# Kernel tuning notes

Measured on AMD Instinct MI355X. Metric: run time of the kernel, lower is better.

The kernel has to match this reference:

```python
import jax, jax.numpy as jnp
import numpy as np

B, S, H, E, K, NH = 2, 2048, 1024, 8, 2, 8
HD = H // NH          # head dim = 128
HQ = H // 4           # seasonal encoder width = 256
CAP = int(B * S * 1.5 * K / E)  # expert capacity = 1536


def setup_inputs() -> dict:
    key = jax.random.key(0)
    ks = iter(jax.random.split(key, 32))

    def lin(shape):
        fan_in = shape[0]
        return jax.random.normal(next(ks), shape, jnp.float32) / np.sqrt(fan_in)

    inp = {
        "hidden_states": jax.random.normal(next(ks), (B, S, H), jnp.float32),
        # position embedding table [sequence_length, H]
        "pos_emb": jax.random.normal(next(ks), (S, H), jnp.float32) * 0.02,
        # temporal_encoder: Linear(H+2,H) -> ReLU -> Linear(H,H)
        "We1": lin((H + 2, H)), "be1": jnp.zeros((H,), jnp.float32),
        "We2": lin((H, H)),     "be2": jnp.zeros((H,), jnp.float32),
        # seasonal_encoder: Linear(1,H//4) -> ReLU -> Linear(H//4,H//4)
        "Ws1": lin((1, HQ)),   "bs1": jnp.zeros((HQ,), jnp.float32),
        "Ws2": lin((HQ, HQ)),  "bs2": jnp.zeros((HQ,), jnp.float32),
        # temporal_attention (MultiheadAttention, 8 heads)
        "Wq": lin((H, H)), "bq": jnp.zeros((H,), jnp.float32),
        "Wk": lin((H, H)), "bk": jnp.zeros((H,), jnp.float32),
        "Wv": lin((H, H)), "bv": jnp.zeros((H,), jnp.float32),
        "Wo": lin((H, H)), "bo": jnp.zeros((H,), jnp.float32),
        # temporal_router: Linear(H,H) -> ReLU -> Linear(H,E)
        "Wr1": lin((H, H)), "br1": jnp.zeros((H,), jnp.float32),
        "Wr2": lin((H, E)), "br2": jnp.zeros((E,), jnp.float32),
    }
    return inp


def _forward(hidden_states, pos_emb, We1, be1, We2, be2, Ws1, bs1, Ws2, bs2,
             Wq, bq, Wk, bk, Wv, bv, Wo, bo, Wr1, br1, Wr2, br2):
    b, s, h = hidden_states.shape
    # time features (time_info is None -> defaults)
    t = jnp.arange(s, dtype=jnp.float32)                   # [S]
    season = jnp.sin(t * 2.0 * jnp.pi / 24.0)              # [S]
    time_feat = jnp.broadcast_to(jnp.stack([t, season], -1), (b, s, 2))

    combined = jnp.concatenate([hidden_states, time_feat], axis=-1)  # [B,S,H+2]
    enc = jax.nn.relu(combined @ We1 + be1) @ We2 + be2              # [B,S,H]

    pos = pos_emb[:s]                                                # [S,H]
    seas = jax.nn.relu(season[:, None] @ Ws1 + bs1) @ Ws2 + bs2      # [S,H//4]
    seas_full = jnp.tile(seas, (1, h // seas.shape[-1]))             # [S,H] (expand to H)

    x = enc + pos[None] + seas_full[None]                            # [B,S,H]

    # self-attention (eval mode, no dropout)
    def heads(y):
        return y.reshape(b, s, NH, HD)
    q = heads(x @ Wq + bq)
    k = heads(x @ Wk + bk)
    v = heads(x @ Wv + bv)
    scores = jnp.einsum('bqhd,bkhd->bhqk', q, k) / np.sqrt(HD)
    attn = jax.nn.softmax(scores, axis=-1)
    ctx = jnp.einsum('bhqk,bkhd->bqhd', attn, v).reshape(b, s, h)
    x = ctx @ Wo + bo

    logits = jax.nn.relu(x @ Wr1 + br1) @ Wr2 + br2                  # [B,S,E]
    probs = jax.nn.softmax(logits, axis=-1)

    topv, topi = jax.lax.top_k(probs, K)                             # [B,S,K]
    topv = topv / topv.sum(-1, keepdims=True)

    onehot = jax.nn.one_hot(topi, E, dtype=probs.dtype)              # [B,S,K,E]
    disp0 = onehot.sum(-2)                                           # [B,S,E] (0/1)
    comb0 = (topv[..., None] * onehot).sum(-2)                       # [B,S,E]

    # only capacity slot 0 is ever written (per original code)
    dispatch = jnp.zeros((b, s, E, CAP), probs.dtype).at[..., 0].set(disp0)
    combine = jnp.zeros((b, s, E, CAP), probs.dtype).at[..., 0].set(comb0)

    p_mean = probs.mean(axis=(0, 1))                                 # [E]
    aux_loss = jnp.sum(p_mean * jnp.log(p_mean * E + 1e-9))
    return dispatch, combine, probs, aux_loss


def reference(hidden_states, pos_emb, We1, be1, We2, be2, Ws1, bs1, Ws2, bs2,
              Wq, bq, Wk, bk, Wv, bv, Wo, bo, Wr1, br1, Wr2, br2):
    return _forward(hidden_states, pos_emb, We1, be1, We2, be2, Ws1, bs1, Ws2, bs2,
                    Wq, bq, Wk, bk, Wv, bv, Wo, bo, Wr1, br1, Wr2, br2)
```

## Files before the change

### kernel.cpp

```cpp
#include <hip/hip_runtime.h>
#include <hip/hip_fp16.h>
#include <math.h>

#define N_TOK 4096
#define S_LEN 2048
#define H_DIM 1024
#define E_EXP 8
#define CAPV  1536
#define NHEAD 8
#define HDHD  128

#define SCRATCH_F4 2129920u
#define TOTAL_F4   25165824u

typedef __attribute__((ext_vector_type(8))) _Float16 v8h;
typedef __attribute__((ext_vector_type(4))) float v4f;

__device__ __forceinline__ void splitf16(float v, unsigned short& h, unsigned short& l) {
    __half hh = __float2half(v);
    h = __half_as_ushort(hh);
    l = __half_as_ushort(__float2half(v - __half2float(hh)));
}

__device__ __forceinline__ void gld_lds16(const void* g, void* l) {
    __builtin_amdgcn_global_load_lds(
        (const __attribute__((address_space(1))) unsigned int*)g,
        (__attribute__((address_space(3))) unsigned int*)l,
        16, 0, 0);
}

__global__ __launch_bounds__(256) void prep_k(
    const float* __restrict__ hid, unsigned short* __restrict__ hi,
    unsigned short* __restrict__ lo,
    const float* __restrict__ Ws1, const float* __restrict__ bs1,
    const float* __restrict__ Ws2, const float* __restrict__ bs2,
    float* __restrict__ seasons, float* __restrict__ seas24,
    const float* __restrict__ Wr2, float* __restrict__ wr2t) {
    __shared__ float hbuf[256];
    int blk = blockIdx.x;
    int tid = threadIdx.x;
    if (blk < 4096) {
        int i = blk * 256 + tid;
        float4 v = ((const float4*)hid)[i];
        ushort4 h, l;
        splitf16(v.x, h.x, l.x);
        splitf16(v.y, h.y, l.y);
        splitf16(v.z, h.z, l.z);
        splitf16(v.w, h.w, l.w);
        ((ushort4*)hi)[i] = h;
        ((ushort4*)lo)[i] = l;
    } else if (blk < 4104) {
        int s = (blk - 4096) * 256 + tid;
        if (s < S_LEN) {
            double a = (double)s * 2.0 * M_PI / 24.0;
            seasons[s] = (float)sin(a);
        }
    } else if (blk < 4128) {
        int m = blk - 4104;
        double a = (double)m * 2.0 * M_PI / 24.0;
        float sv = (float)sin(a);
        int j = tid;
        hbuf[j] = fmaxf(sv * Ws1[j] + bs1[j], 0.f);
        __syncthreads();
        float acc = bs2[j];
        for (int i = 0; i < 256; ++i) acc = fmaf(hbuf[i], Ws2[i * 256 + j], acc);
        seas24[m * 256 + j] = acc;
    } else {
        int i = (blk - 4128) * 256 + tid;
        int k = i >> 3, e = i & 7;
        wr2t[e * 1024 + k] = Wr2[i];
    }
}

__device__ __forceinline__ void wconv_body(const float* __restrict__ W,
                                           unsigned short* __restrict__ Thi,
                                           unsigned short* __restrict__ Tlo) {
    __shared__ unsigned short Hs[64][65];
    __shared__ unsigned short Ls[64][65];
    int k0 = blockIdx.y * 64, n0 = blockIdx.x * 64;
    int tid = threadIdx.x;
#pragma unroll
    for (int i = 0; i < 4; ++i) {
        int idx = tid + i * 256;
        int kk = idx >> 4, n4 = idx & 15;
        float4 v = *(const float4*)(W + (size_t)(k0 + kk) * 1024 + n0 + n4 * 4);
        unsigned short h, l;
        splitf16(v.x, h, l); Hs[n4 * 4 + 0][kk] = h; Ls[n4 * 4 + 0][kk] = l;
        splitf16(v.y, h, l); Hs[n4 * 4 + 1][kk] = h; Ls[n4 * 4 + 1][kk] = l;
        splitf16(v.z, h, l); Hs[n4 * 4 + 2][kk] = h; Ls[n4 * 4 + 2][kk] = l;
        splitf16(v.w, h, l); Hs[n4 * 4 + 3][kk] = h; Ls[n4 * 4 + 3][kk] = l;
    }
    __syncthreads();
#pragma unroll
    for (int i = 0; i < 4; ++i) {
        int idx = tid + i * 256;
        int n = idx >> 4, k4 = idx & 15;
        ushort4 h = make_ushort4(Hs[n][k4 * 4], Hs[n][k4 * 4 + 1], Hs[n][k4 * 4 + 2], Hs[n][k4 * 4 + 3]);
        ushort4 l = make_ushort4(Ls[n][k4 * 4], Ls[n][k4 * 4 + 1], Ls[n][k4 * 4 + 2], Ls[n][k4 * 4 + 3]);
        *(ushort4*)(Thi + (size_t)(n0 + n) * 1024 + k0 + k4 * 4) = h;
        *(ushort4*)(Tlo + (size_t)(n0 + n) * 1024 + k0 + k4 * 4) = l;
    }
}

struct WBatch {
    const float* src[7];
    unsigned short* dh[7];
    unsigned short* dl[7];
};

__global__ __launch_bounds__(256) void wconv_batch_k(WBatch wb) {
    int i = blockIdx.z;
    wconv_body(wb.src[i], wb.dh[i], wb.dl[i]);
}

__device__ __forceinline__ void fill_body(float* __restrict__ p, size_t f40, size_t f41, int nblk) {
    v4f z = {0.f, 0.f, 0.f, 0.f};
    v4f* o = (v4f*)p;
    size_t n = f41 - f40;
    size_t T = blockDim.x;
    for (size_t i = (size_t)blockIdx.x * T + threadIdx.x; i < n; i += (size_t)nblk * T)
        __builtin_nontemporal_store(z, o + f40 + i);
}

template <int MODE, int EMITF, int EMITS, int FILLN>
__global__ __launch_bounds__(512, 4) void gemm_split(
    const unsigned short* __restrict__ Ahi, const unsigned short* __restrict__ Alo,
    const unsigned short* __restrict__ WThi, const unsigned short* __restrict__ WTlo,
    const float* __restrict__ bias, float* __restrict__ Cf,
    unsigned short* __restrict__ Chi, unsigned short* __restrict__ Clo,
    const float* __restrict__ rowT, const float* __restrict__ rowS,
    const float* __restrict__ seasons, const float* __restrict__ pos,
    const float* __restrict__ seas24, float escale, float* __restrict__ fillp) {
    if (FILLN > 0) {
        if (blockIdx.x < (unsigned)FILLN) {
            fill_body(fillp, 0, SCRATCH_F4, FILLN);
            return;
        }
    }
    __shared__ unsigned short Ash[2][128 * 32];
    __shared__ unsigned short Asl[2][128 * 32];
    __shared__ unsigned short Bsh[2][128 * 32];
    __shared__ unsigned short Bsl[2][128 * 32];
    int tid = threadIdx.x;
    int lane = tid & 63, w = tid >> 6;
    int l15 = lane & 15, l16 = lane >> 4;
    int wm = (w >> 1) * 32, wn = (w & 1) * 64;

    int bid = blockIdx.x - FILLN;
    int mp = (bid & 7) + ((bid >> 6) << 3);
    int np = (bid >> 3) & 7;
    int m0 = mp * 128, n0 = np * 128;

    int ac0 = tid;
    int ar0 = ac0 >> 2;
    size_t a_src0 = (size_t)(m0 + ar0) * 1024 + (((ac0 & 3) ^ (ar0 & 3)) * 8);
    size_t b_src0 = (size_t)(n0 + ar0) * 1024 + (((ac0 & 3) ^ (ar0 & 3)) * 8);

    int a_off[2], b_off[4];
#pragma unroll
    for (int mi = 0; mi < 2; ++mi) {
        int row = wm + mi * 16 + l15;
        a_off[mi] = row * 32 + ((l16 ^ (row & 3)) * 8);
    }
#pragma unroll
    for (int ni = 0; ni < 4; ++ni) {
        int n = wn + ni * 16 + l15;
        b_off[ni] = n * 32 + ((l16 ^ (n & 3)) * 8);
    }

    auto STAGE = [&](int buf, int k0) {
        gld_lds16(Ahi + a_src0 + k0, &Ash[buf][ac0 * 8]);
        gld_lds16(Alo + a_src0 + k0, &Asl[buf][ac0 * 8]);
        gld_lds16(WThi + b_src0 + k0, &Bsh[buf][ac0 * 8]);
        gld_lds16(WTlo + b_src0 + k0, &Bsl[buf][ac0 * 8]);
    };

    v4f acc[2][4] = {};
    STAGE(0, 0);
    __syncthreads();

    for (int kk = 0; kk < 32; ++kk) {
        int cur = kk & 1;
        if (kk < 31) STAGE(cur ^ 1, (kk + 1) * 32);
        v8h ah[2], al[2], bh[4], bl[4];
#pragma unroll
        for (int mi = 0; mi < 2; ++mi) {
            ah[mi] = *(const v8h*)&Ash[cur][a_off[mi]];
            al[mi] = *(const v8h*)&Asl[cur][a_off[mi]];
        }
#pragma unroll
        for (int ni = 0; ni < 4; ++ni) {
            bh[ni] = *(const v8h*)&Bsh[cur][b_off[ni]];
            bl[ni] = *(const v8h*)&Bsl[cur][b_off[ni]];
        }
#pragma unroll
        for (int mi = 0; mi < 2; ++mi)
#pragma unroll
            for (int ni = 0; ni < 4; ++ni) {
                acc[mi][ni] = __builtin_amdgcn_mfma_f32_16x16x32_f16(ah[mi], bh[ni], acc[mi][ni], 0, 0, 0);
                acc[mi][ni] = __builtin_amdgcn_mfma_f32_16x16x32_f16(al[mi], bh[ni], acc[mi][ni], 0, 0, 0);
                acc[mi][ni] = __builtin_amdgcn_mfma_f32_16x16x32_f16(ah[mi], bl[ni], acc[mi][ni], 0, 0, 0);
            }
        __syncthreads();
    }

#pragma unroll
    for (int mi = 0; mi < 2; ++mi) {
#pragma unroll
        for (int r = 0; r < 4; ++r) {
            int row = m0 + wm + mi * 16 + l16 * 4 + r;
            int s = row & (S_LEN - 1);
            float tval = 0.f, seval = 0.f;
            if (MODE == 1) { tval = (float)s; seval = seasons[s]; }
#pragma unroll
            for (int ni = 0; ni < 4; ++ni) {
                int col = n0 + wn + ni * 16 + l15;
                float v = acc[mi][ni][r] + bias[col];
                if (MODE == 1) v += tval * rowT[col] + seval * rowS[col];
                if (MODE == 2) v += pos[(size_t)s * 1024 + col] + seas24[(s % 24) * 256 + (col & 255)];
                if (MODE == 1 || MODE == 3) v = fmaxf(v, 0.f);
                size_t o = (size_t)row * 1024 + col;
                if (EMITF) Cf[o] = v;
                if (EMITS) {
                    unsigned short hu, lu;
                    splitf16(v * escale, hu, lu);
                    Chi[o] = hu; Clo[o] = lu;
                }
            }
        }
    }
}

#define NFILLQ 128
__global__ __launch_bounds__(512, 4) void gemm_qkv(
    const unsigned short* __restrict__ Ahi, const unsigned short* __restrict__ Alo,
    const unsigned short* __restrict__ WT3hi, const unsigned short* __restrict__ WT3lo,
    const float* __restrict__ bq, const float* __restrict__ bk,
    const float* __restrict__ bv,
    unsigned short* __restrict__ Qhi, unsigned short* __restrict__ Qlo,
    unsigned short* __restrict__ Khi, unsigned short* __restrict__ Klo,
    unsigned short* __restrict__ VThi, unsigned short* __restrict__ VTlo,
    float qscale, float* __restrict__ fillp) {
    if (blockIdx.x < NFILLQ) {
        fill_body(fillp, SCRATCH_F4, TOTAL_F4, NFILLQ);
        return;
    }
    __shared__ unsigned short Ash[2][128 * 32];
    __shared__ unsigned short Asl[2][128 * 32];
    __shared__ unsigned short Bsh[2][128 * 32];
    __shared__ unsigned short Bsl[2][128 * 32];
    int tid = threadIdx.x;
    int lane = tid & 63, w = tid >> 6;
    int l15 = lane & 15, l16 = lane >> 4;
    int wm = (w >> 1) * 32, wn = (w & 1) * 64;

    int bid = blockIdx.x - NFILLQ;
    int t = bid >> 3;
    int np = t % 24;
    int mp = (bid & 7) + (t / 24) * 8;
    int m0 = mp * 128;
    int wn0 = np * 128;

    int ac0 = tid;
    int ar0 = ac0 >> 2;
    size_t a_src0 = (size_t)(m0 + ar0) * 1024 + (((ac0 & 3) ^ (ar0 & 3)) * 8);
    size_t b_src0 = (size_t)(wn0 + ar0) * 1024 + (((ac0 & 3) ^ (ar0 & 3)) * 8);

    int a_off[2], b_off[4];
#pragma unroll
    for (int mi = 0; mi < 2; ++mi) {
        int row = wm + mi * 16 + l15;
        a_off[mi] = row * 32 + ((l16 ^ (row & 3)) * 8);
    }
#pragma unroll
    for (int ni = 0; ni < 4; ++ni) {
        int n = wn + ni * 16 + l15;
        b_off[ni] = n * 32 + ((l16 ^ (n & 3)) * 8);
    }

    auto STAGE = [&](int buf, int k0) {
        gld_lds16(Ahi + a_src0 + k0, &Ash[buf][ac0 * 8]);
        gld_lds16(Alo + a_src0 + k0, &Asl[buf][ac0 * 8]);
        gld_lds16(WT3hi + b_src0 + k0, &Bsh[buf][ac0 * 8]);
        gld_lds16(WT3lo + b_src0 + k0, &Bsl[buf][ac0 * 8]);
    };

    v4f acc[2][4] = {};
    STAGE(0, 0);
    __syncthreads();

    for (int kk = 0; kk < 32; ++kk) {
        int cur = kk & 1;
        if (kk < 31) STAGE(cur ^ 1, (kk + 1) * 32);
        v8h ah[2], al[2], bh[4], bl[4];
#pragma unroll
        for (int mi = 0; mi < 2; ++mi) {
            ah[mi] = *(const v8h*)&Ash[cur][a_off[mi]];
            al[mi] = *(const v8h*)&Asl[cur][a_off[mi]];
        }
#pragma unroll
        for (int ni = 0; ni < 4; ++ni) {
            bh[ni] = *(const v8h*)&Bsh[cur][b_off[ni]];
            bl[ni] = *(const v8h*)&Bsl[cur][b_off[ni]];
        }
#pragma unroll
        for (int mi = 0; mi < 2; ++mi)
#pragma unroll
            for (int ni = 0; ni < 4; ++ni) {
                acc[mi][ni] = __builtin_amdgcn_mfma_f32_16x16x32_f16(ah[mi], bh[ni], acc[mi][ni], 0, 0, 0);
                acc[mi][ni] = __builtin_amdgcn_mfma_f32_16x16x32_f16(al[mi], bh[ni], acc[mi][ni], 0, 0, 0);
                acc[mi][ni] = __builtin_amdgcn_mfma_f32_16x16x32_f16(ah[mi], bl[ni], acc[mi][ni], 0, 0, 0);
            }
        __syncthreads();
    }

    if (np >= 16) {
        int n0 = (np - 16) * 128;
#pragma unroll
        for (int mi = 0; mi < 2; ++mi) {
            int row0 = m0 + wm + mi * 16 + l16 * 4;
            int bb = row0 >> 11, ss = row0 & 2047;
#pragma unroll
            for (int ni = 0; ni < 4; ++ni) {
                int col = n0 + wn + ni * 16 + l15;
                int hh = col >> 7, dd = col & 127;
                size_t base = ((size_t)((bb * 8 + hh) * 128 + dd)) * 2048 + ss;
                ushort4 vh, vl;
                float v0 = acc[mi][ni][0] + bv[col];
                float v1 = acc[mi][ni][1] + bv[col];
                float v2 = acc[mi][ni][2] + bv[col];
                float v3 = acc[mi][ni][3] + bv[col];
                splitf16(v0, vh.x, vl.x);
                splitf16(v1, vh.y, vl.y);
                splitf16(v2, vh.z, vl.z);
                splitf16(v3, vh.w, vl.w);
                *(ushort4*)(VThi + base) = vh;
                *(ushort4*)(VTlo + base) = vl;
            }
        }
    } else {
        const float* bias = np < 8 ? bq : bk;
        unsigned short* Dhi = np < 8 ? Qhi : Khi;
        unsigned short* Dlo = np < 8 ? Qlo : Klo;
        float esc = np < 8 ? qscale : 1.f;
        int n0 = (np & 7) * 128;
#pragma unroll
        for (int mi = 0; mi < 2; ++mi) {
#pragma unroll
            for (int r = 0; r < 4; ++r) {
                int row = m0 + wm + mi * 16 + l16 * 4 + r;
#pragma unroll
                for (int ni = 0; ni < 4; ++ni) {
                    int col = n0 + wn + ni * 16 + l15;
                    float v = (acc[mi][ni][r] + bias[col]) * esc;
                    size_t o = (size_t)row * 1024 + col;
                    unsigned short hu, lu;
                    splitf16(v, hu, lu);
                    Dhi[o] = hu; Dlo[o] = lu;
                }
            }
        }
    }
}

__global__ __launch_bounds__(256, 4) void attn_mfma_k(
    const unsigned short* __restrict__ qhi, const unsigned short* __restrict__ qlo,
    const unsigned short* __restrict__ khi, const unsigned short* __restrict__ klo,
    const unsigned short* __restrict__ vthi, const unsigned short* __restrict__ vtlo,
    float* __restrict__ OP, float* __restrict__ ML) {
    __shared__ unsigned short Ks_hi[32 * 128];
    __shared__ unsigned short Ks_lo[32 * 128];
    __shared__ unsigned short Vs_hi[128 * 32];
    __shared__ unsigned short Vs_lo[128 * 32];
    __shared__ unsigned int   Ps[64 * 32];

    int p = blockIdx.x;
    int x = (p >> 3) & 31;
    int g = (p & 7) + ((p >> 8) << 3);
    int bh = g >> 1, z = g & 1;
    int b = bh >> 3, h = bh & 7;
    int q0 = x * 64;
    int tid = threadIdx.x;
    int lane = tid & 63, w = tid >> 6;
    int l15 = lane & 15, l16 = lane >> 4;
    int wm = w * 16;

    v8h qa_h[4], qa_l[4];
    {
        size_t qrow = (size_t)(b * S_LEN + q0 + wm + l15) * H_DIM + h * HDHD;
#pragma unroll
        for (int ks = 0; ks < 4; ++ks) {
            qa_h[ks] = *(const v8h*)(qhi + qrow + ks * 32 + l16 * 8);
            qa_l[ks] = *(const v8h*)(qlo + qrow + ks * 32 + l16 * 8);
        }
    }

    int ktok1 = tid >> 4, kslot1 = tid & 15;
    int ktok2 = ktok1 + 16;
    size_t ksrc1 = (size_t)(b * S_LEN + ktok1) * H_DIM + h * HDHD + ((kslot1 ^ (ktok1 & 7)) * 8);
    size_t ksrc2 = (size_t)(b * S_LEN + ktok2) * H_DIM + h * HDHD + ((kslot1 ^ (ktok2 & 7)) * 8);
    int vd1 = tid >> 2, vslot1 = tid & 3;
    int vd2 = vd1 + 64;
    size_t vsrc1 = (size_t)(bh * HDHD + vd1) * S_LEN + ((vslot1 ^ ((vd1 >> 1) & 3)) * 8);
    size_t vsrc2 = (size_t)(bh * HDHD + vd2) * S_LEN + ((vslot1 ^ ((vd2 >> 1) & 3)) * 8);

    v4f accO[8] = {};
    float mreg[4] = {-1e30f, -1e30f, -1e30f, -1e30f};
    float lreg[4] = {};

    int kt0 = z * 1024;
    for (int it = 0; it < 32; ++it) {
        int kt = kt0 + it * 32;
        __syncthreads();
        size_t koff = (size_t)kt * H_DIM;
        gld_lds16(khi + ksrc1 + koff, &Ks_hi[tid * 8]);
        gld_lds16(khi + ksrc2 + koff, &Ks_hi[(tid + 256) * 8]);
        gld_lds16(klo + ksrc1 + koff, &Ks_lo[tid * 8]);
        gld_lds16(klo + ksrc2 + koff, &Ks_lo[(tid + 256) * 8]);
        gld_lds16(vthi + vsrc1 + kt, &Vs_hi[tid * 8]);
        gld_lds16(vthi + vsrc2 + kt, &Vs_hi[(tid + 256) * 8]);
        gld_lds16(vtlo + vsrc1 + kt, &Vs_lo[tid * 8]);
        gld_lds16(vtlo + vsrc2 + kt, &Vs_lo[(tid + 256) * 8]);
        __syncthreads();

        v4f s0 = {}, s1 = {};
#pragma unroll
        for (int ks = 0; ks < 4; ++ks) {
#pragma unroll
            for (int nt = 0; nt < 2; ++nt) {
                int tok = nt * 16 + l15;
                int slot = (ks * 4 + l16) ^ (tok & 7);
                v8h bhf = *(const v8h*)&Ks_hi[tok * 128 + slot * 8];
                v8h blf = *(const v8h*)&Ks_lo[tok * 128 + slot * 8];
                v4f& ss = nt ? s1 : s0;
                ss = __builtin_amdgcn_mfma_f32_16x16x32_f16(qa_h[ks], bhf, ss, 0, 0, 0);
                ss = __builtin_amdgcn_mfma_f32_16x16x32_f16(qa_l[ks], bhf, ss, 0, 0, 0);
                ss = __builtin_amdgcn_mfma_f32_16x16x32_f16(qa_h[ks], blf, ss, 0, 0, 0);
            }
        }

        float p0[4], p1[4], alpha[4];
#pragma unroll
        for (int r = 0; r < 4; ++r) {
            float tmax = fmaxf(s0[r], s1[r]);
            tmax = fmaxf(tmax, __shfl_xor(tmax, 1));
            tmax = fmaxf(tmax, __shfl_xor(tmax, 2));
            tmax = fmaxf(tmax, __shfl_xor(tmax, 4));
            tmax = fmaxf(tmax, __shfl_xor(tmax, 8));
            float mnew = fmaxf(mreg[r], tmax);
            alpha[r] = __expf(mreg[r] - mnew);
            p0[r] = __expf(s0[r] - mnew);
            p1[r] = __expf(s1[r] - mnew);
            float lt = p0[r] + p1[r];
            lt += __shfl_xor(lt, 1);
            lt += __shfl_xor(lt, 2);
            lt += __shfl_xor(lt, 4);
            lt += __shfl_xor(lt, 8);
            lreg[r] = lreg[r] * alpha[r] + lt;
            mreg[r] = mnew;
        }
#pragma unroll
        for (int nt = 0; nt < 8; ++nt)
#pragma unroll
            for (int r = 0; r < 4; ++r) accO[nt][r] *= alpha[r];

#pragma unroll
        for (int r = 0; r < 4; ++r) {
            int qq = wm + l16 * 4 + r;
            unsigned short ph, pl;
            splitf16(p0[r], ph, pl);
            int k0i = l15;
            Ps[qq * 32 + ((((k0i >> 2) ^ (qq & 7)) << 2) | (k0i & 3))] =
                (unsigned)ph | ((unsigned)pl << 16);
            splitf16(p1[r], ph, pl);
            int k1i = 16 + l15;
            Ps[qq * 32 + ((((k1i >> 2) ^ (qq & 7)) << 2) | (k1i & 3))] =
                (unsigned)ph | ((unsigned)pl << 16);
        }

        int qq = wm + l15;
        int sA = (l16 * 2) ^ (qq & 7);
        int sB = (l16 * 2 + 1) ^ (qq & 7);
        uint4 ua = *(const uint4*)&Ps[qq * 32 + sA * 4];
        uint4 ub = *(const uint4*)&Ps[qq * 32 + sB * 4];
        uint4 ahw, alw;
        ahw.x = (ua.x & 0xffffu) | (ua.y << 16);
        ahw.y = (ua.z & 0xffffu) | (ua.w << 16);
        ahw.z = (ub.x & 0xffffu) | (ub.y << 16);
        ahw.w = (ub.z & 0xffffu) | (ub.w << 16);
        alw.x = (ua.x >> 16) | (ua.y & 0xffff0000u);
        alw.y = (ua.z >> 16) | (ua.w & 0xffff0000u);
        alw.z = (ub.x >> 16) | (ub.y & 0xffff0000u);
        alw.w = (ub.z >> 16) | (ub.w & 0xffff0000u);
        v8h pA_h = __builtin_bit_cast(v8h, ahw);
        v8h pA_l = __builtin_bit_cast(v8h, alw);
#pragma unroll
        for (int nt = 0; nt < 8; ++nt) {
            int d = nt * 16 + l15;
            int slot = l16 ^ ((d >> 1) & 3);
            v8h vhf = *(const v8h*)&Vs_hi[d * 32 + slot * 8];
            v8h vlf = *(const v8h*)&Vs_lo[d * 32 + slot * 8];
            accO[nt] = __builtin_amdgcn_mfma_f32_16x16x32_f16(pA_h, vhf, accO[nt], 0, 0, 0);
            accO[nt] = __builtin_amdgcn_mfma_f32_16x16x32_f16(pA_l, vhf, accO[nt], 0, 0, 0);
            accO[nt] = __builtin_amdgcn_mfma_f32_16x16x32_f16(pA_h, vlf, accO[nt], 0, 0, 0);
        }
    }

#pragma unroll
    for (int r = 0; r < 4; ++r) {
        if (l15 == 0) {
            int q = q0 + wm + l16 * 4 + r;
            size_t mlo = ((size_t)(z * 16 + bh) * 2048 + q) * 2;
            ML[mlo] = mreg[r];
            ML[mlo + 1] = lreg[r];
        }
    }
#pragma unroll
    for (int nt = 0; nt < 8; ++nt) {
#pragma unroll
        for (int r = 0; r < 4; ++r) {
            int q = q0 + wm + l16 * 4 + r;
            size_t o = ((size_t)(z * 16 + bh) * 2048 + q) * 128 + nt * 16 + l15;
            OP[o] = accO[nt][r];
        }
    }
}

__global__ __launch_bounds__(256) void attn_combine_k(
    const float* __restrict__ OP, const float* __restrict__ ML,
    unsigned short* __restrict__ ctx_hi, unsigned short* __restrict__ ctx_lo) {
    int tid = threadIdx.x;
    int R = blockIdx.x * 16 + (tid >> 4);
    int bh = R >> 11, q = R & 2047;
    int b = bh >> 3, h = bh & 7;
    int d0 = (tid & 15) * 8;
    size_t ml0 = ((size_t)bh * 2048 + q) * 2;
    size_t ml1 = ((size_t)(16 + bh) * 2048 + q) * 2;
    float m0 = ML[ml0], l0 = ML[ml0 + 1];
    float m1 = ML[ml1], l1 = ML[ml1 + 1];
    float m = fmaxf(m0, m1);
    float w0 = __expf(m0 - m), w1 = __expf(m1 - m);
    float inv = 1.f / (w0 * l0 + w1 * l1);
    const float* O0 = OP + ((size_t)bh * 2048 + q) * 128 + d0;
    const float* O1 = OP + ((size_t)(16 + bh) * 2048 + q) * 128 + d0;
    size_t dst = ((size_t)(b * 2048 + q)) * 1024 + h * 128 + d0;
    float4 a0 = *(const float4*)O0;
    float4 a1 = *(const float4*)(O0 + 4);
    float4 c0 = *(const float4*)O1;
    float4 c1 = *(const float4*)(O1 + 4);
    ushort4 h0, h1, lo0, lo1;
    splitf16((w0 * a0.x + w1 * c0.x) * inv, h0.x, lo0.x);
    splitf16((w0 * a0.y + w1 * c0.y) * inv, h0.y, lo0.y);
    splitf16((w0 * a0.z + w1 * c0.z) * inv, h0.z, lo0.z);
    splitf16((w0 * a0.w + w1 * c0.w) * inv, h0.w, lo0.w);
    splitf16((w0 * a1.x + w1 * c1.x) * inv, h1.x, lo1.x);
    splitf16((w0 * a1.y + w1 * c1.y) * inv, h1.y, lo1.y);
    splitf16((w0 * a1.z + w1 * c1.z) * inv, h1.z, lo1.z);
    splitf16((w0 * a1.w + w1 * c1.w) * inv, h1.w, lo1.w);
    *(ushort4*)(ctx_hi + dst) = h0;
    *(ushort4*)(ctx_hi + dst + 4) = h1;
    *(ushort4*)(ctx_lo + dst) = lo0;
    *(ushort4*)(ctx_lo + dst + 4) = lo1;
}

__global__ __launch_bounds__(256) void logits_topk_k(const float* __restrict__ h1,
                                                     const float* __restrict__ Wr2T,
                                                     const float* __restrict__ br2,
                                                     float* __restrict__ out) {
    __shared__ float part[256];
    __shared__ float lg[8][8];
    int tid = threadIdx.x;
    int tok8 = tid >> 5;
    int e = (tid >> 2) & 7;
    int ch = tid & 3;
    int tok = blockIdx.x * 8 + tok8;
    const float4* h4 = (const float4*)(h1 + (size_t)tok * 1024 + ch * 256);
    const float4* w4 = (const float4*)(Wr2T + (size_t)e * 1024 + ch * 256);
    float acc = 0.f;
#pragma unroll
    for (int i = 0; i < 64; ++i) {
        float4 a = h4[i];
        float4 bb = w4[i];
        acc = fmaf(a.x, bb.x, fmaf(a.y, bb.y, fmaf(a.z, bb.z, fmaf(a.w, bb.w, acc))));
    }
    part[tid] = acc;
    __syncthreads();
    if (ch == 0)
        lg[tok8][e] = part[tid] + part[tid + 1] + part[tid + 2] + part[tid + 3] + br2[e];
    __syncthreads();
    if (tid < 8) {
        int myTok = blockIdx.x * 8 + tid;
        float l[8], p[8];
        float mx = -1e30f;
#pragma unroll
        for (int k = 0; k < 8; ++k) { l[k] = lg[tid][k]; mx = fmaxf(mx, l[k]); }
        float sum = 0.f;
#pragma unroll
        for (int k = 0; k < 8; ++k) { p[k] = __expf(l[k] - mx); sum += p[k]; }
        float inv = 1.f / sum;
#pragma unroll
        for (int k = 0; k < 8; ++k) p[k] *= inv;
        const size_t NEC = (size_t)N_TOK * E_EXP * CAPV;
        float* probs_out = out + 2 * NEC;
#pragma unroll
        for (int k = 0; k < 8; ++k) probs_out[(size_t)myTok * 8 + k] = p[k];
        int i1 = 0;
#pragma unroll
        for (int k = 1; k < 8; ++k) if (p[k] > p[i1]) i1 = k;
        int i2 = -1;
#pragma unroll
        for (int k = 0; k < 8; ++k) {
            if (k == i1) continue;
            if (i2 < 0 || p[k] > p[i2]) i2 = k;
        }
        float v1 = p[i1], v2 = p[i2], tv = v1 + v2;
        size_t base = (size_t)myTok * E_EXP * CAPV;
        out[base + (size_t)i1 * CAPV] = 1.f;
        out[base + (size_t)i2 * CAPV] = 1.f;
        out[NEC + base + (size_t)i1 * CAPV] = v1 / tv;
        out[NEC + base + (size_t)i2 * CAPV] = v2 / tv;
    }
}

__global__ void aux_k(const float* __restrict__ probs, float* __restrict__ out_aux) {
    __shared__ float part[256];
    int tid = threadIdx.x;
    int e = tid & 7, chunk = tid >> 3;
    float s = 0.f;
    for (int t = chunk * 128; t < (chunk + 1) * 128; ++t)
        s += probs[(size_t)t * 8 + e];
    part[tid] = s;
    __syncthreads();
    if (tid < 8) {
        float tot = 0.f;
        for (int c = 0; c < 32; ++c) tot += part[c * 8 + e];
        part[tid] = tot / (float)N_TOK;
    }
    __syncthreads();
    if (tid == 0) {
        float aux = 0.f;
        for (int e2 = 0; e2 < 8; ++e2) {
            float pm = part[e2];
            aux += pm * logf(pm * 8.f + 1e-9f);
        }
        *out_aux = aux;
    }
}

extern "C" void kernel_launch(void* const* d_in, const int* in_sizes, int n_in,
                              void* d_out, int out_size, void* d_ws, size_t ws_size,
                              hipStream_t stream) {
    const float* hid = (const float*)d_in[0];
    const float* pos = (const float*)d_in[1];
    const float* We1 = (const float*)d_in[2];
    const float* be1 = (const float*)d_in[3];
    const float* We2 = (const float*)d_in[4];
    const float* be2 = (const float*)d_in[5];
    const float* Ws1 = (const float*)d_in[6];
    const float* bs1 = (const float*)d_in[7];
    const float* Ws2 = (const float*)d_in[8];
    const float* bs2 = (const float*)d_in[9];
    const float* Wq  = (const float*)d_in[10]; const float* bq = (const float*)d_in[11];
    const float* Wk  = (const float*)d_in[12]; const float* bk = (const float*)d_in[13];
    const float* Wv  = (const float*)d_in[14]; const float* bv = (const float*)d_in[15];
    const float* Wo  = (const float*)d_in[16]; const float* bo = (const float*)d_in[17];
    const float* Wr1 = (const float*)d_in[18]; const float* br1 = (const float*)d_in[19];
    const float* Wr2 = (const float*)d_in[20]; const float* br2 = (const float*)d_in[21];

    float* out = (float*)d_out;
    char* base = (char*)d_ws;
    const size_t AC  = (size_t)N_TOK * H_DIM;
    const size_t SPC = AC * 2;
    const size_t FB  = AC * 4;
    const size_t MB  = (size_t)1 << 20;

    unsigned short* B1hi = (unsigned short*)(base);
    unsigned short* B1lo = (unsigned short*)(base + SPC);
    unsigned short* B2hi = (unsigned short*)(base + FB);
    unsigned short* B2lo = (unsigned short*)(base + FB + SPC);
    unsigned short* Qhi  = (unsigned short*)(base + 2 * FB);
    unsigned short* Qlo  = (unsigned short*)(base + 2 * FB + SPC);
    unsigned short* Khi  = (unsigned short*)(base + 3 * FB);
    unsigned short* Klo  = (unsigned short*)(base + 3 * FB + SPC);
    unsigned short* VThi = (unsigned short*)(base + 4 * FB);
    unsigned short* VTlo = (unsigned short*)(base + 4 * FB + SPC);
    float* h1f = (float*)(base + 3 * FB);

    char* wp = base + 5 * FB;
    unsigned short* We1hi = (unsigned short*)(wp);
    unsigned short* We1lo = (unsigned short*)(wp + 2 * MB);
    unsigned short* We2hi = (unsigned short*)(wp + 4 * MB);
    unsigned short* We2lo = (unsigned short*)(wp + 6 * MB);
    unsigned short* QKVhi = (unsigned short*)(wp + 8 * MB);
    unsigned short* QKVlo = (unsigned short*)(wp + 14 * MB);
    unsigned short* Wohi  = (unsigned short*)(wp + 20 * MB);
    unsigned short* Wolo  = (unsigned short*)(wp + 22 * MB);
    unsigned short* Wr1hi = (unsigned short*)(wp + 24 * MB);
    unsigned short* Wr1lo = (unsigned short*)(wp + 26 * MB);
    char* smalls = wp + 28 * MB;
    float* wr2t    = (float*)smalls;
    float* seas24  = wr2t + 8192;
    float* seasons = seas24 + 6144;

    const size_t NEC = (size_t)N_TOK * E_EXP * CAPV;
    const float QSCALE = 0.08838834764831845f;

    float* OP = out;
    float* ML = out + (size_t)2 * 16 * 2048 * 128;

    dim3 blk(256), blk512(512);

    prep_k<<<4160, blk, 0, stream>>>(hid, B1hi, B1lo, Ws1, bs1, Ws2, bs2,
                                     seasons, seas24, Wr2, wr2t);

    WBatch wb;
    wb.src[0] = We1; wb.dh[0] = We1hi; wb.dl[0] = We1lo;
    wb.src[1] = We2; wb.dh[1] = We2hi; wb.dl[1] = We2lo;
    wb.src[2] = Wq;  wb.dh[2] = QKVhi;                        wb.dl[2] = QKVlo;
    wb.src[3] = Wk;  wb.dh[3] = QKVhi + (size_t)1024 * 1024;  wb.dl[3] = QKVlo + (size_t)1024 * 1024;
    wb.src[4] = Wv;  wb.dh[4] = QKVhi + (size_t)2048 * 1024;  wb.dl[4] = QKVlo + (size_t)2048 * 1024;
    wb.src[5] = Wo;  wb.dh[5] = Wohi;  wb.dl[5] = Wolo;
    wb.src[6] = Wr1; wb.dh[6] = Wr1hi; wb.dl[6] = Wr1lo;
    wconv_batch_k<<<dim3(16, 16, 7), blk, 0, stream>>>(wb);

    gemm_split<1, 0, 1, 0><<<256, blk512, 0, stream>>>(B1hi, B1lo, We1hi, We1lo, be1,
        nullptr, B2hi, B2lo,
        We1 + (size_t)1024 * 1024, We1 + (size_t)1025 * 1024, seasons, nullptr, nullptr, 1.f, nullptr);
    gemm_split<2, 0, 1, 0><<<256, blk512, 0, stream>>>(B2hi, B2lo, We2hi, We2lo, be2,
        nullptr, B1hi, B1lo, nullptr, nullptr, nullptr, pos, seas24, 1.f, nullptr);

    gemm_qkv<<<768 + NFILLQ, blk512, 0, stream>>>(B1hi, B1lo, QKVhi, QKVlo, bq, bk, bv,
                                                  Qhi, Qlo, Khi, Klo, VThi, VTlo, QSCALE, out);

    attn_mfma_k<<<1024, blk, 0, stream>>>(Qhi, Qlo, Khi, Klo, VThi, VTlo, OP, ML);
    attn_combine_k<<<2048, blk, 0, stream>>>(OP, ML, B2hi, B2lo);

    gemm_split<0, 0, 1, 32><<<256 + 32, blk512, 0, stream>>>(B2hi, B2lo, Wohi, Wolo, bo,
        nullptr, B1hi, B1lo, nullptr, nullptr, nullptr, nullptr, nullptr, 1.f, out);
    gemm_split<3, 1, 0, 0><<<256, blk512, 0, stream>>>(B1hi, B1lo, Wr1hi, Wr1lo, br1,
        h1f, nullptr, nullptr, nullptr, nullptr, nullptr, nullptr, nullptr, 1.f, nullptr);

    logits_topk_k<<<512, blk, 0, stream>>>(h1f, wr2t, br2, out);
    aux_k<<<1, blk, 0, stream>>>(out + 2 * NEC, out + 2 * NEC + (size_t)N_TOK * E_EXP);
}
```

Before: 523.6 us.

## Merge prep and weight-conversion kernels; enlarge attention query tile to 128

Folds the weight hi/lo split-and-transpose blocks into the prep kernel so both run in a single launch, removing one kernel boundary. The attention kernel now runs 512-thread blocks covering 128 query rows, so each K/V tile staged in LDS is shared by twice as many query rows and each thread issues half as many async loads. The trade-off is fewer blocks (512), lower occupancy per launch bound, and a larger P buffer in shared memory.

```diff
diff --git a/kernel.cpp b/kernel.cpp
--- a/kernel.cpp
+++ b/kernel.cpp
@@ -29,14 +29,21 @@
         16, 0, 0);
 }
 
-__global__ __launch_bounds__(256) void prep_k(
+struct WBatch {
+    const float* src[7];
+    unsigned short* dh[7];
+    unsigned short* dl[7];
+};
+
+__global__ __launch_bounds__(256) void prep_wconv_k(
     const float* __restrict__ hid, unsigned short* __restrict__ hi,
     unsigned short* __restrict__ lo,
     const float* __restrict__ Ws1, const float* __restrict__ bs1,
     const float* __restrict__ Ws2, const float* __restrict__ bs2,
     float* __restrict__ seasons, float* __restrict__ seas24,
-    const float* __restrict__ Wr2, float* __restrict__ wr2t) {
-    __shared__ float hbuf[256];
+    const float* __restrict__ Wr2, float* __restrict__ wr2t, WBatch wb) {
+    __shared__ unsigned short Hs[64][65];
+    __shared__ unsigned short Ls[64][65];
     int blk = blockIdx.x;
     int tid = threadIdx.x;
     if (blk < 4096) {
@@ -56,6 +63,7 @@
             seasons[s] = (float)sin(a);
         }
     } else if (blk < 4128) {
+        float* hbuf = (float*)Hs;
         int m = blk - 4104;
         double a = (double)m * 2.0 * M_PI / 24.0;
         float sv = (float)sin(a);
@@ -65,52 +73,40 @@
         float acc = bs2[j];
         for (int i = 0; i < 256; ++i) acc = fmaf(hbuf[i], Ws2[i * 256 + j], acc);
         seas24[m * 256 + j] = acc;
-    } else {
+    } else if (blk < 4160) {
         int i = (blk - 4128) * 256 + tid;
         int k = i >> 3, e = i & 7;
         wr2t[e * 1024 + k] = Wr2[i];
-    }
-}
-
-__device__ __forceinline__ void wconv_body(const float* __restrict__ W,
-                                           unsigned short* __restrict__ Thi,
-                                           unsigned short* __restrict__ Tlo) {
-    __shared__ unsigned short Hs[64][65];
-    __shared__ unsigned short Ls[64][65];
-    int k0 = blockIdx.y * 64, n0 = blockIdx.x * 64;
-    int tid = threadIdx.x;
-#pragma unroll
-    for (int i = 0; i < 4; ++i) {
-        int idx = tid + i * 256;
-        int kk = idx >> 4, n4 = idx & 15;
-        float4 v = *(const float4*)(W + (size_t)(k0 + kk) * 1024 + n0 + n4 * 4);
-        unsigned short h, l;
-        splitf16(v.x, h, l); Hs[n4 * 4 + 0][kk] = h; Ls[n4 * 4 + 0][kk] = l;
-        splitf16(v.y, h, l); Hs[n4 * 4 + 1][kk] = h; Ls[n4 * 4 + 1][kk] = l;
-        splitf16(v.z, h, l); Hs[n4 * 4 + 2][kk] = h; Ls[n4 * 4 + 2][kk] = l;
-        splitf16(v.w, h, l); Hs[n4 * 4 + 3][kk] = h; Ls[n4 * 4 + 3][kk] = l;
-    }
-    __syncthreads();
-#pragma unroll
-    for (int i = 0; i < 4; ++i) {
-        int idx = tid + i * 256;
-        int n = idx >> 4, k4 = idx & 15;
-        ushort4 h = make_ushort4(Hs[n][k4 * 4], Hs[n][k4 * 4 + 1], Hs[n][k4 * 4 + 2], Hs[n][k4 * 4 + 3]);
-        ushort4 l = make_ushort4(Ls[n][k4 * 4], Ls[n][k4 * 4 + 1], Ls[n][k4 * 4 + 2], Ls[n][k4 * 4 + 3]);
-        *(ushort4*)(Thi + (size_t)(n0 + n) * 1024 + k0 + k4 * 4) = h;
-        *(ushort4*)(Tlo + (size_t)(n0 + n) * 1024 + k0 + k4 * 4) = l;
-    }
-}
-
-struct WBatch {
-    const float* src[7];
-    unsigned short* dh[7];
-    unsigned short* dl[7];
-};
-
-__global__ __launch_bounds__(256) void wconv_batch_k(WBatch wb) {
-    int i = blockIdx.z;
-    wconv_body(wb.src[i], wb.dh[i], wb.dl[i]);
+    } else {
+        int i2 = blk - 4160;
+        int wi = i2 >> 8;
+        int rem = i2 & 255;
+        int k0 = (rem >> 4) << 6, n0 = (rem & 15) << 6;
+        const float* __restrict__ W = wb.src[wi];
+        unsigned short* __restrict__ Thi = wb.dh[wi];
+        unsigned short* __restrict__ Tlo = wb.dl[wi];
+#pragma unroll
+        for (int i = 0; i < 4; ++i) {
+            int idx = tid + i * 256;
+            int kk = idx >> 4, n4 = idx & 15;
+            float4 v = *(const float4*)(W + (size_t)(k0 + kk) * 1024 + n0 + n4 * 4);
+            unsigned short h, l;
+            splitf16(v.x, h, l); Hs[n4 * 4 + 0][kk] = h; Ls[n4 * 4 + 0][kk] = l;
+            splitf16(v.y, h, l); Hs[n4 * 4 + 1][kk] = h; Ls[n4 * 4 + 1][kk] = l;
+            splitf16(v.z, h, l); Hs[n4 * 4 + 2][kk] = h; Ls[n4 * 4 + 2][kk] = l;
+            splitf16(v.w, h, l); Hs[n4 * 4 + 3][kk] = h; Ls[n4 * 4 + 3][kk] = l;
+        }
+        __syncthreads();
+#pragma unroll
+        for (int i = 0; i < 4; ++i) {
+            int idx = tid + i * 256;
+            int n = idx >> 4, k4 = idx & 15;
+            ushort4 h = make_ushort4(Hs[n][k4 * 4], Hs[n][k4 * 4 + 1], Hs[n][k4 * 4 + 2], Hs[n][k4 * 4 + 3]);
+            ushort4 l = make_ushort4(Ls[n][k4 * 4], Ls[n][k4 * 4 + 1], Ls[n][k4 * 4 + 2], Ls[n][k4 * 4 + 3]);
+            *(ushort4*)(Thi + (size_t)(n0 + n) * 1024 + k0 + k4 * 4) = h;
+            *(ushort4*)(Tlo + (size_t)(n0 + n) * 1024 + k0 + k4 * 4) = l;
+        }
+    }
 }
 
 __device__ __forceinline__ void fill_body(float* __restrict__ p, size_t f40, size_t f41, int nblk) {
@@ -363,7 +359,7 @@
     }
 }
 
-__global__ __launch_bounds__(256, 4) void attn_mfma_k(
+__global__ __launch_bounds__(512, 2) void attn_mfma_k(
     const unsigned short* __restrict__ qhi, const unsigned short* __restrict__ qlo,
     const unsigned short* __restrict__ khi, const unsigned short* __restrict__ klo,
     const unsigned short* __restrict__ vthi, const unsigned short* __restrict__ vtlo,
@@ -372,14 +368,14 @@
     __shared__ unsigned short Ks_lo[32 * 128];
     __shared__ unsigned short Vs_hi[128 * 32];
     __shared__ unsigned short Vs_lo[128 * 32];
-    __shared__ unsigned int   Ps[64 * 32];
+    __shared__ unsigned int   Ps[128 * 32];
 
     int p = blockIdx.x;
-    int x = (p >> 3) & 31;
-    int g = (p & 7) + ((p >> 8) << 3);
+    int x = (p >> 3) & 15;
+    int g = (p & 7) + ((p >> 7) << 3);
     int bh = g >> 1, z = g & 1;
     int b = bh >> 3, h = bh & 7;
-    int q0 = x * 64;
+    int q0 = x * 128;
     int tid = threadIdx.x;
     int lane = tid & 63, w = tid >> 6;
     int l15 = lane & 15, l16 = lane >> 4;
@@ -395,14 +391,10 @@
         }
     }
 
-    int ktok1 = tid >> 4, kslot1 = tid & 15;
-    int ktok2 = ktok1 + 16;
-    size_t ksrc1 = (size_t)(b * S_LEN + ktok1) * H_DIM + h * HDHD + ((kslot1 ^ (ktok1 & 7)) * 8);
-    size_t ksrc2 = (size_t)(b * S_LEN + ktok2) * H_DIM + h * HDHD + ((kslot1 ^ (ktok2 & 7)) * 8);
-    int vd1 = tid >> 2, vslot1 = tid & 3;
-    int vd2 = vd1 + 64;
-    size_t vsrc1 = (size_t)(bh * HDHD + vd1) * S_LEN + ((vslot1 ^ ((vd1 >> 1) & 3)) * 8);
-    size_t vsrc2 = (size_t)(bh * HDHD + vd2) * S_LEN + ((vslot1 ^ ((vd2 >> 1) & 3)) * 8);
+    int ktok = tid >> 4, kslot = tid & 15;
+    size_t ksrc = (size_t)(b * S_LEN + ktok) * H_DIM + h * HDHD + ((kslot ^ (ktok & 7)) * 8);
+    int vd = tid >> 2, vslot = tid & 3;
+    size_t vsrc = (size_t)(bh * HDHD + vd) * S_LEN + ((vslot ^ ((vd >> 1) & 3)) * 8);
 
     v4f accO[8] = {};
     float mreg[4] = {-1e30f, -1e30f, -1e30f, -1e30f};
@@ -413,14 +405,10 @@
         int kt = kt0 + it * 32;
         __syncthreads();
         size_t koff = (size_t)kt * H_DIM;
-        gld_lds16(khi + ksrc1 + koff, &Ks_hi[tid * 8]);
-        gld_lds16(khi + ksrc2 + koff, &Ks_hi[(tid + 256) * 8]);
-        gld_lds16(klo + ksrc1 + koff, &Ks_lo[tid * 8]);
-        gld_lds16(klo + ksrc2 + koff, &Ks_lo[(tid + 256) * 8]);
-        gld_lds16(vthi + vsrc1 + kt, &Vs_hi[tid * 8]);
-        gld_lds16(vthi + vsrc2 + kt, &Vs_hi[(tid + 256) * 8]);
-        gld_lds16(vtlo + vsrc1 + kt, &Vs_lo[tid * 8]);
-        gld_lds16(vtlo + vsrc2 + kt, &Vs_lo[(tid + 256) * 8]);
+        gld_lds16(khi + ksrc + koff, &Ks_hi[tid * 8]);
+        gld_lds16(klo + ksrc + koff, &Ks_lo[tid * 8]);
+        gld_lds16(vthi + vsrc + kt, &Vs_hi[tid * 8]);
+        gld_lds16(vtlo + vsrc + kt, &Vs_lo[tid * 8]);
         __syncthreads();
 
         v4f s0 = {}, s1 = {};
@@ -710,9 +698,6 @@
 
     dim3 blk(256), blk512(512);
 
-    prep_k<<<4160, blk, 0, stream>>>(hid, B1hi, B1lo, Ws1, bs1, Ws2, bs2,
-                                     seasons, seas24, Wr2, wr2t);
-
     WBatch wb;
     wb.src[0] = We1; wb.dh[0] = We1hi; wb.dl[0] = We1lo;
     wb.src[1] = We2; wb.dh[1] = We2hi; wb.dl[1] = We2lo;
@@ -721,7 +706,9 @@
     wb.src[4] = Wv;  wb.dh[4] = QKVhi + (size_t)2048 * 1024;  wb.dl[4] = QKVlo + (size_t)2048 * 1024;
     wb.src[5] = Wo;  wb.dh[5] = Wohi;  wb.dl[5] = Wolo;
     wb.src[6] = Wr1; wb.dh[6] = Wr1hi; wb.dl[6] = Wr1lo;
-    wconv_batch_k<<<dim3(16, 16, 7), blk, 0, stream>>>(wb);
+
+    prep_wconv_k<<<5952, blk, 0, stream>>>(hid, B1hi, B1lo, Ws1, bs1, Ws2, bs2,
+                                           seasons, seas24, Wr2, wr2t, wb);
 
     gemm_split<1, 0, 1, 0><<<256, blk512, 0, stream>>>(B1hi, B1lo, We1hi, We1lo, be1,
         nullptr, B2hi, B2lo,
@@ -732,7 +719,7 @@
     gemm_qkv<<<768 + NFILLQ, blk512, 0, stream>>>(B1hi, B1lo, QKVhi, QKVlo, bq, bk, bv,
                                                   Qhi, Qlo, Khi, Klo, VThi, VTlo, QSCALE, out);
 
-    attn_mfma_k<<<1024, blk, 0, stream>>>(Qhi, Qlo, Khi, Klo, VThi, VTlo, OP, ML);
+    attn_mfma_k<<<512, blk512, 0, stream>>>(Qhi, Qlo, Khi, Klo, VThi, VTlo, OP, ML);
     attn_combine_k<<<2048, blk, 0, stream>>>(OP, ML, B2hi, B2lo);
 
     gemm_split<0, 0, 1, 32><<<256 + 32, blk512, 0, stream>>>(B2hi, B2lo, Wohi, Wolo, bo,
```

New measurement: 540.9 us. +3.3%, slower.
